# Optimization experiments

Hardware: AMD Instinct MI355X
Metric: run time of the kernel (lower is better)

## Reference

```python
import jax, jax.numpy as jnp
import numpy as np

D_MODEL = 128
D_INNER = 256   # expand=2
D_STATE = 16
DT_RANK = 8     # ceil(128/16)
D_CONV = 2
GROUPS = 4
EPS = 1e-5


def _mamba_dir(x, W_in, conv_w, conv_b, W_x, W_dt, b_dt, A_log, D, W_out):
    # x: [B, L, d_model]
    B, L, _ = x.shape
    xz = x @ W_in                               # [B, L, 2*d_inner]
    xp, z = xz[..., :D_INNER], xz[..., D_INNER:]
    # depthwise causal conv, kernel size 2 (pad-left 1)
    xprev = jnp.pad(xp, ((0, 0), (1, 0), (0, 0)))[:, :L]
    xc = jax.nn.silu(xprev * conv_w[:, 0] + xp * conv_w[:, 1] + conv_b)
    xdb = xc @ W_x                              # [B, L, dt_rank + 2*d_state]
    dt_r = xdb[..., :DT_RANK]
    Bc = xdb[..., DT_RANK:DT_RANK + D_STATE]    # [B, L, d_state]
    Cc = xdb[..., DT_RANK + D_STATE:]           # [B, L, d_state]
    dt = jax.nn.softplus(dt_r @ W_dt + b_dt)    # [B, L, d_inner]
    A = -jnp.exp(A_log)                         # [d_inner, d_state]

    def step(h, inp):
        dt_t, B_t, C_t, x_t = inp               # [B,di], [B,ds], [B,ds], [B,di]
        dA = jnp.exp(dt_t[:, :, None] * A)      # [B, di, ds]
        h = dA * h + (dt_t * x_t)[:, :, None] * B_t[:, None, :]
        y = jnp.einsum('bds,bs->bd', h, C_t)
        return h, y

    h0 = jnp.zeros((B, D_INNER, D_STATE), x.dtype)
    xs = (jnp.moveaxis(dt, 1, 0), jnp.moveaxis(Bc, 1, 0),
          jnp.moveaxis(Cc, 1, 0), jnp.moveaxis(xc, 1, 0))
    _, ys = jax.lax.scan(step, h0, xs)          # ys: [L, B, d_inner]
    y = jnp.moveaxis(ys, 0, 1) + D * xc
    y = y * jax.nn.silu(z)
    return y @ W_out                            # [B, L, d_model]


def _groupnorm_silu(x, gamma, beta):
    B, C, H, W = x.shape
    xg = x.reshape(B, GROUPS, C // GROUPS, H, W)
    mu = xg.mean(axis=(2, 3, 4), keepdims=True)
    var = xg.var(axis=(2, 3, 4), keepdims=True)
    xn = ((xg - mu) * jax.lax.rsqrt(var + EPS)).reshape(B, C, H, W)
    return jax.nn.silu(xn * gamma[None, :, None, None] + beta[None, :, None, None])


def setup_inputs() -> dict:
    key = jax.random.key(0)
    ks = jax.random.split(key, 24)
    s = 0.02
    A_log = jnp.log(jnp.tile(jnp.arange(1, D_STATE + 1, dtype=jnp.float32)[None, :], (D_INNER, 1)))
    inp = {"x": jax.random.normal(ks[0], (4, D_MODEL, 64, 64), jnp.float32)}
    for i, sfx in enumerate(("f", "b")):
        o = 1 + 9 * i
        inp[f"W_in_{sfx}"] = jax.random.normal(ks[o], (D_MODEL, 2 * D_INNER)) * s
        inp[f"conv_w_{sfx}"] = jax.random.normal(ks[o + 1], (D_INNER, D_CONV)) * 0.5
        inp[f"conv_b_{sfx}"] = jnp.zeros((D_INNER,))
        inp[f"W_x_{sfx}"] = jax.random.normal(ks[o + 2], (D_INNER, DT_RANK + 2 * D_STATE)) * s
        inp[f"W_dt_{sfx}"] = jax.random.normal(ks[o + 3], (DT_RANK, D_INNER)) * s
        inp[f"b_dt_{sfx}"] = jnp.full((D_INNER,), -3.0)
        inp[f"A_log_{sfx}"] = A_log
        inp[f"D_{sfx}"] = jnp.ones((D_INNER,))
        inp[f"W_out_{sfx}"] = jax.random.normal(ks[o + 4], (D_INNER, D_MODEL)) * s
    inp["gn_gamma"] = jnp.ones((D_MODEL,))
    inp["gn_beta"] = jnp.zeros((D_MODEL,))
    return inp


def reference(x, W_in_f, conv_w_f, conv_b_f, W_x_f, W_dt_f, b_dt_f, A_log_f, D_f, W_out_f,
              W_in_b, conv_w_b, conv_b_b, W_x_b, W_dt_b, b_dt_b, A_log_b, D_b, W_out_b,
              gn_gamma, gn_beta):
    B, C, H, W = x.shape
    xs = x.transpose(0, 2, 3, 1).reshape(B, H * W, C)
    y_f = _mamba_dir(xs, W_in_f, conv_w_f, conv_b_f, W_x_f, W_dt_f, b_dt_f, A_log_f, D_f, W_out_f)
    xr = xs[:, ::-1]
    y_b = _mamba_dir(xr, W_in_b, conv_w_b, conv_b_b, W_x_b, W_dt_b, b_dt_b, A_log_b, D_b, W_out_b)[:, ::-1]
    y = y_f + y_b                               # bidirectional combine
    y = y.reshape(B, H, W, C).transpose(0, 3, 1, 2)
    y = _groupnorm_silu(y, gn_gamma, gn_beta)
    return y + x
```

## Files before the change

### kernel.cpp

```cpp
#include <hip/hip_runtime.h>

#define Bn 4
#define Ln 4096
#define Cn 128
#define DIn 256
#define NCn 128
#define LCn 32
#define ROWS (Bn*Ln)

typedef short s8v __attribute__((ext_vector_type(8)));
typedef short s4v __attribute__((ext_vector_type(4)));
typedef unsigned short u8v __attribute__((ext_vector_type(8)));
typedef unsigned short u4v __attribute__((ext_vector_type(4)));
typedef float f4v __attribute__((ext_vector_type(4)));
typedef float f2v __attribute__((ext_vector_type(2)));

__device__ __forceinline__ float siluf(float x){ return x / (1.f + __expf(-x)); }
__device__ __forceinline__ unsigned short bfr(float f){
  uint u = __float_as_uint(f);
  return (unsigned short)((u + 0x7fffu + ((u>>16)&1u)) >> 16);
}
__device__ __forceinline__ float bf2f(unsigned short u){ return __uint_as_float(((uint)u)<<16); }

__device__ __forceinline__ void sp_w(float r, float& dtv, float& w){
  float e = __expf(-fabsf(r));
  float rc = 1.f / (1.f + e);
  dtv = fmaxf(r, 0.f) + __logf(1.f + e);
  w = (r > 0.f) ? e * rc : rc;
}

__device__ __forceinline__ int tile_off(int r, int gran, int ghalf){
  return ((r>>4)<<9) + ((r&15)<<5) + (((gran ^ ((r>>1)&3)))<<3) + ghalf;
}

#define SMEMB 18432

__global__ __launch_bounds__(256) void k_g1(const float* __restrict__ x,
    const float* __restrict__ Wf, const float* __restrict__ Wb,
    unsigned short* __restrict__ xpf, unsigned short* __restrict__ xpb,
    unsigned short* __restrict__ zbf, unsigned short* __restrict__ zbb)
{
  const int dir = blockIdx.z;
  const float* __restrict__ W = dir ? Wb : Wf;
  unsigned short* __restrict__ xp = dir ? xpb : xpf;
  unsigned short* __restrict__ zb = dir ? zbb : zbf;
  const int row0 = blockIdx.x * 128;
  const int n0 = blockIdx.y;
  const int b = row0 >> 12;
  const int t0 = row0 & (Ln-1);
  const float* __restrict__ xb = x + (size_t)b * Cn * Ln;

  __shared__ __align__(16) char smem[SMEMB];
  short* Ast = (short*)smem;
  short* Bst = (short*)smem + 8*512;
  float* Te  = (float*)smem;

  const int tid = threadIdx.x;
  const int lane = tid & 63;
  const int wid = tid >> 6;
  const int wr = wid >> 1, wc = wid & 1;
  const int r16 = lane & 15, kg = lane >> 4;

  const int q = tid & 31, kq = tid >> 5;
  const int kbase = 4*kq;
  const int g_true = kq >> 1;
  const int ghalf = (kq & 1) * 4;

  f4v acc[4][4];
  #pragma unroll
  for (int i=0;i<4;++i)
    #pragma unroll
    for (int j=0;j<4;++j) acc[i][j] = (f4v){0.f,0.f,0.f,0.f};

  float4 va[4], vb[4];
  {
    #pragma unroll
    for (int kk=0;kk<4;++kk) {
      va[kk] = (dir==0)
        ? *(const float4*)(xb + (size_t)(kbase+kk)*Ln + t0 + 4*q)
        : *(const float4*)(xb + (size_t)(kbase+kk)*Ln + (Ln-4 - t0 - 4*q));
      vb[kk] = *(const float4*)(W + (size_t)(kbase+kk)*512 + n0*128 + 4*q);
    }
  }
  for (int ks=0; ks<4; ++ks) {
    if (ks) __syncthreads();
    #pragma unroll
    for (int e=0;e<4;++e) {
      int r = 4*q + e;
      int off = tile_off(r, g_true, ghalf);
      int c = dir ? (3-e) : e;
      s4v hv;
      #pragma unroll
      for (int kk=0;kk<4;++kk) hv[kk] = (short)bfr(((const float*)&va[kk])[c]);
      *(s4v*)&Ast[off] = hv;
    }
    #pragma unroll
    for (int e=0;e<4;++e) {
      int r = 4*q + e;
      int off = tile_off(r, g_true, ghalf);
      s4v hv;
      #pragma unroll
      for (int kk=0;kk<4;++kk) hv[kk] = (short)bfr(((const float*)&vb[kk])[e]);
      *(s4v*)&Bst[off] = hv;
    }
    __syncthreads();
    if (ks < 3) {
      const int k0n = (ks+1)*32;
      #pragma unroll
      for (int kk=0;kk<4;++kk) {
        va[kk] = (dir==0)
          ? *(const float4*)(xb + (size_t)(k0n+kbase+kk)*Ln + t0 + 4*q)
          : *(const float4*)(xb + (size_t)(k0n+kbase+kk)*Ln + (Ln-4 - t0 - 4*q));
        vb[kk] = *(const float4*)(W + (size_t)(k0n+kbase+kk)*512 + n0*128 + 4*q);
      }
    }
    const int gsh = ((kg ^ ((r16>>1)&3)) << 3);
    s8v fa[4], fb[4];
    #pragma unroll
    for (int m=0;m<4;++m) fa[m] = *(const s8v*)&Ast[(wr*4+m)*512 + r16*32 + gsh];
    #pragma unroll
    for (int n=0;n<4;++n) fb[n] = *(const s8v*)&Bst[(wc*4+n)*512 + r16*32 + gsh];
    #pragma unroll
    for (int m=0;m<4;++m)
      #pragma unroll
      for (int n=0;n<4;++n)
        acc[m][n] = __builtin_amdgcn_mfma_f32_16x16x32_bf16(fa[m], fb[n], acc[m][n], 0,0,0);
  }
  __syncthreads();
  float* Tw = Te + wid*1088;
  #pragma unroll
  for (int m=0;m<4;++m) {
    #pragma unroll
    for (int n=0;n<4;++n)
      #pragma unroll
      for (int v=0;v<4;++v)
        Tw[(kg*4+v)*68 + n*16 + r16] = acc[m][n][v];
    #pragma unroll
    for (int rr=0;rr<4;++rr) {
      int r = rr*4 + (lane>>4);
      int c4 = lane & 15;
      float4 v4 = *(const float4*)&Tw[r*68 + c4*4];
      int row = row0 + wr*64 + m*16 + r;
      int colL = wc*64 + c4*4;
      u4v u; u[0]=bfr(v4.x); u[1]=bfr(v4.y); u[2]=bfr(v4.z); u[3]=bfr(v4.w);
      if (n0 < 2) {
        *(u4v*)(xp + (size_t)row*256 + n0*128 + colL) = u;
      } else {
        *(u4v*)(zb + (size_t)row*256 + (n0-2)*128 + colL) = u;
      }
    }
  }
}

__global__ __launch_bounds__(256) void k_conv(
    const unsigned short* __restrict__ xpf, const unsigned short* __restrict__ xpb,
    const float* __restrict__ cwf, const float* __restrict__ cwb,
    const float* __restrict__ cbf, const float* __restrict__ cbb,
    unsigned short* __restrict__ xcf, unsigned short* __restrict__ xcb)
{
  const int dir = blockIdx.y;
  const unsigned short* __restrict__ xpd = dir ? xpb : xpf;
  const float* __restrict__ cw = dir ? cwb : cwf;
  const float* __restrict__ cb = dir ? cbb : cbf;
  unsigned short* __restrict__ xc = dir ? xcb : xcf;
  const int n4 = ROWS * 64;
  for (int idx4 = blockIdx.x*256 + threadIdx.x; idx4 < n4; idx4 += gridDim.x*256) {
    int row = idx4 >> 6;
    int d0 = (idx4 & 63) * 4;
    u4v curu = *(const u4v*)(xpd + (size_t)row*256 + d0);
    u4v prevu = (u4v){0,0,0,0};
    if (row & (Ln-1)) prevu = *(const u4v*)(xpd + (size_t)(row-1)*256 + d0);
    float4 cwA = *(const float4*)(cw + d0*2);
    float4 cwB = *(const float4*)(cw + d0*2 + 4);
    float4 cb4 = *(const float4*)(cb + d0);
    u4v r;
    r[0] = bfr(siluf(fmaf(bf2f(prevu[0]),cwA.x, fmaf(bf2f(curu[0]),cwA.y, cb4.x))));
    r[1] = bfr(siluf(fmaf(bf2f(prevu[1]),cwA.z, fmaf(bf2f(curu[1]),cwA.w, cb4.y))));
    r[2] = bfr(siluf(fmaf(bf2f(prevu[2]),cwB.x, fmaf(bf2f(curu[2]),cwB.y, cb4.z))));
    r[3] = bfr(siluf(fmaf(bf2f(prevu[3]),cwB.z, fmaf(bf2f(curu[3]),cwB.w, cb4.w))));
    *(u4v*)(xc + (size_t)row*256 + d0) = r;
  }
}

__global__ __launch_bounds__(256) void k_g2(
    const unsigned short* __restrict__ xcf, const unsigned short* __restrict__ xcb,
    const float* __restrict__ Wxf, const float* __restrict__ Wxb,
    float* __restrict__ xdbf, float* __restrict__ xdbb)
{
  const int dir = blockIdx.z;
  const unsigned short* __restrict__ xc = dir ? xcb : xcf;
  const float* __restrict__ Wx = dir ? Wxb : Wxf;
  float* __restrict__ xdb = dir ? xdbb : xdbf;
  const int row0 = blockIdx.x * 64;

  __shared__ __align__(16) short Ast[4*512];
  __shared__ __align__(16) short Bst[4*512];

  const int tid = threadIdx.x;
  const int lane = tid & 63;
  const int wid = tid >> 6;
  const int wr = wid >> 1, wc = wid & 1;
  const int r16 = lane & 15, kg = lane >> 4;
  const int ar = tid >> 2, ag = tid & 3;
  const int bn = tid & 63, bg = tid >> 6;

  f4v acc[2][2];
  #pragma unroll
  for (int i=0;i<2;++i)
    #pragma unroll
    for (int j=0;j<2;++j) acc[i][j] = (f4v){0.f,0.f,0.f,0.f};

  for (int ks=0; ks<8; ++ks) {
    const int k0 = ks*32;
    if (ks) __syncthreads();
    {
      u8v u = *(const u8v*)(xc + (size_t)(row0+ar)*256 + k0 + ag*8);
      *(u8v*)&Ast[tile_off(ar, ag, 0)] = u;
    }
    {
      s8v hv;
      #pragma unroll
      for (int i=0;i<8;++i) {
        int k = k0 + bg*8 + i;
        float f = (bn < 40) ? Wx[(size_t)k*40 + bn] : 0.f;
        hv[i] = (short)bfr(f);
      }
      *(s8v*)&Bst[tile_off(bn, bg, 0)] = hv;
    }
    __syncthreads();
    const int gsh = ((kg ^ ((r16>>1)&3)) << 3);
    s8v fa[2], fb[2];
    #pragma unroll
    for (int m=0;m<2;++m) fa[m] = *(const s8v*)&Ast[(wr*2+m)*512 + r16*32 + gsh];
    #pragma unroll
    for (int n=0;n<2;++n) fb[n] = *(const s8v*)&Bst[(wc*2+n)*512 + r16*32 + gsh];
    #pragma unroll
    for (int m=0;m<2;++m)
      #pragma unroll
      for (int n=0;n<2;++n)
        acc[m][n] = __builtin_amdgcn_mfma_f32_16x16x32_bf16(fa[m], fb[n], acc[m][n], 0,0,0);
  }
  #pragma unroll
  for (int m=0;m<2;++m)
    #pragma unroll
    for (int n=0;n<2;++n) {
      int col = wc*32 + n*16 + r16;
      if (col < 40) {
        #pragma unroll
        for (int v=0;v<4;++v) {
          int row = row0 + wr*32 + m*16 + kg*4 + v;
          xdb[(size_t)row*40 + col] = acc[m][n][v];
        }
      }
    }
}

__global__ __launch_bounds__(128,4) void k_pass1(
    const float* __restrict__ xdbf, const float* __restrict__ xdbb,
    const unsigned short* __restrict__ xcf, const unsigned short* __restrict__ xcb,
    const float* __restrict__ Wdtf, const float* __restrict__ Wdtb,
    const float* __restrict__ bdtf, const float* __restrict__ bdtb,
    const float* __restrict__ Alf, const float* __restrict__ Alb,
    float* __restrict__ sdtf, float* __restrict__ sdtb,
    float* __restrict__ hkf, float* __restrict__ hkb)
{
  const int dir = blockIdx.y;
  const float* __restrict__ xdb = dir ? xdbb : xdbf;
  const unsigned short* __restrict__ xc = dir ? xcb : xcf;
  const float* __restrict__ Wdt = dir ? Wdtb : Wdtf;
  const float* __restrict__ bdt = dir ? bdtb : bdtf;
  const float* __restrict__ Al  = dir ? Alb  : Alf;
  float* __restrict__ sdt = dir ? sdtb : sdtf;
  float* __restrict__ hk  = dir ? hkb  : hkf;
  const int dh = blockIdx.x & 1;
  const int cc = blockIdx.x >> 1;
  const int b = cc >> 7, c = cc & 127;
  const int t0 = c * LCn;
  __shared__ float S[LCn*32];
  const int tid = threadIdx.x;
  #pragma unroll
  for (int j=0;j<6;++j) {
    int idx = tid + j*128;
    int t = idx/24, jj = idx - t*24;
    S[t*32 + jj] = xdb[(size_t)(b*Ln + t0 + t)*40 + jj];
  }
  const int d = dh*128 + tid;
  float Areg[16];
  bool st = true;
  #pragma unroll
  for (int s=0;s<16;++s) {
    Areg[s] = -__expf(Al[d*16+s]);
    st = st && (fabsf(Areg[s] + (float)(s+1)) <= 3e-5f*(float)(s+1));
  }
  f2v wdt2[4];
  #pragma unroll
  for (int j=0;j<4;++j) wdt2[j] = (f2v){Wdt[(2*j)*256+d], Wdt[(2*j+1)*256+d]};
  const float bd = bdt[d];
  f2v h2[8];
  #pragma unroll
  for (int i=0;i<8;++i) h2[i] = (f2v){0.f,0.f};
  float sacc = 0.f;
  const unsigned short* xcp = xc + (size_t)(b*Ln + t0)*256 + d;
  __syncthreads();
  if (st) {
    for (int t=0;t<LCn;++t) {
      float4 sA = *(const float4*)&S[t*32];
      float4 sB = *(const float4*)&S[t*32+4];
      f2v r2 = (f2v){sA.x,sA.y}*wdt2[0] + (f2v){sA.z,sA.w}*wdt2[1];
      r2 = (f2v){sB.x,sB.y}*wdt2[2] + r2;
      r2 = (f2v){sB.z,sB.w}*wdt2[3] + r2;
      float rr = bd + r2.x + r2.y;
      float dtv, wv;
      sp_w(rr, dtv, wv);
      float4 b0 = *(const float4*)&S[t*32+8];
      float4 b1 = *(const float4*)&S[t*32+12];
      float4 b2 = *(const float4*)&S[t*32+16];
      float4 b3 = *(const float4*)&S[t*32+20];
      float xv = bf2f(xcp[(size_t)t*256]);
      float u = dtv * xv;
      sacc += dtv;
      float w2s = wv*wv;
      float w4 = w2s*w2s, w8 = w4*w4;
      f2v wstep = (f2v){w2s, w2s};
      f2v wpa = (f2v){wv, w2s};
      f2v wpb = wpa * (f2v){w8, w8};
      f2v u2 = (f2v){u, u};
      h2[0] = h2[0]*wpa + u2*(f2v){b0.x,b0.y}; wpa *= wstep;
      h2[4] = h2[4]*wpb + u2*(f2v){b2.x,b2.y}; wpb *= wstep;
      h2[1] = h2[1]*wpa + u2*(f2v){b0.z,b0.w}; wpa *= wstep;
      h2[5] = h2[5]*wpb + u2*(f2v){b2.z,b2.w}; wpb *= wstep;
      h2[2] = h2[2]*wpa + u2*(f2v){b1.x,b1.y}; wpa *= wstep;
      h2[6] = h2[6]*wpb + u2*(f2v){b3.x,b3.y}; wpb *= wstep;
      h2[3] = h2[3]*wpa + u2*(f2v){b1.z,b1.w};
      h2[7] = h2[7]*wpb + u2*(f2v){b3.z,b3.w};
    }
  } else {
    for (int t=0;t<LCn;++t) {
      float4 sA = *(const float4*)&S[t*32];
      float4 sB = *(const float4*)&S[t*32+4];
      float rr = bd;
      rr = fmaf(sA.x,wdt2[0].x, fmaf(sA.y,wdt2[0].y, fmaf(sA.z,wdt2[1].x, fmaf(sA.w,wdt2[1].y, rr))));
      rr = fmaf(sB.x,wdt2[2].x, fmaf(sB.y,wdt2[2].y, fmaf(sB.z,wdt2[3].x, fmaf(sB.w,wdt2[3].y, rr))));
      float dtv, wv;
      sp_w(rr, dtv, wv);
      float bq[16];
      #pragma unroll
      for (int i=0;i<4;++i) *(float4*)&bq[4*i] = *(const float4*)&S[t*32 + 8 + 4*i];
      float xv = bf2f(xcp[(size_t)t*256]);
      float u = dtv * xv;
      sacc += dtv;
      #pragma unroll
      for (int s=0;s<16;++s) {
        float hv = (s&1) ? h2[s>>1].y : h2[s>>1].x;
        hv = fmaf(hv, __expf(dtv*Areg[s]), u*bq[s]);
        if (s&1) h2[s>>1].y = hv; else h2[s>>1].x = hv;
      }
    }
  }
  sdt[(size_t)(b*NCn + c)*256 + d] = sacc;
  #pragma unroll
  for (int i=0;i<8;++i) {
    hk[(size_t)((b*NCn + c)*16 + 2*i)*256 + d]   = h2[i].x;
    hk[(size_t)((b*NCn + c)*16 + 2*i+1)*256 + d] = h2[i].y;
  }
}

__global__ __launch_bounds__(256) void k_pass2(
    const float* __restrict__ Alf, const float* __restrict__ Alb,
    const float* __restrict__ sdtf, const float* __restrict__ sdtb,
    float* __restrict__ hkf, float* __restrict__ hkb)
{
  const int dir = blockIdx.y;
  const float* __restrict__ Al  = dir ? Alb : Alf;
  const float* __restrict__ sdt = dir ? sdtb : sdtf;
  float* __restrict__ hk = dir ? hkb : hkf;
  int g = blockIdx.x*256 + threadIdx.x;
  int d = g & 255, s = (g >> 8) & 15, b = g >> 12;
  float Ad = -__expf(Al[d*16+s]);
  float h = 0.f;
  float sd_n = sdt[(size_t)(b*NCn)*256 + d];
  size_t hi_n = (size_t)((b*NCn)*16 + s)*256 + d;
  float he_n = hk[hi_n];
  for (int c=0;c<NCn;++c) {
    float sd = sd_n, he = he_n;
    size_t hi = hi_n;
    if (c+1 < NCn) {
      int bc = b*NCn + c + 1;
      sd_n = sdt[(size_t)bc*256 + d];
      hi_n = (size_t)(bc*16 + s)*256 + d;
      he_n = hk[hi_n];
    }
    hk[hi] = h;
    h = fmaf(__expf(Ad*sd), h, he);
  }
}

__global__ __launch_bounds__(128,4) void k_pass3(
    const float* __restrict__ xdbf, const float* __restrict__ xdbb,
    const unsigned short* __restrict__ xcf, const unsigned short* __restrict__ xcb,
    const float* __restrict__ Wdtf, const float* __restrict__ Wdtb,
    const float* __restrict__ bdtf, const float* __restrict__ bdtb,
    const float* __restrict__ Alf, const float* __restrict__ Alb,
    const float* __restrict__ Dvf, const float* __restrict__ Dvb,
    const float* __restrict__ hkf, const float* __restrict__ hkb,
    const unsigned short* __restrict__ zbf, const unsigned short* __restrict__ zbb,
    unsigned short* __restrict__ ygf, unsigned short* __restrict__ ygb)
{
  const int dir = blockIdx.y;
  const float* __restrict__ xdb = dir ? xdbb : xdbf;
  const unsigned short* __restrict__ xc = dir ? xcb : xcf;
  const float* __restrict__ Wdt = dir ? Wdtb : Wdtf;
  const float* __restrict__ bdt = dir ? bdtb : bdtf;
  const float* __restrict__ Al  = dir ? Alb  : Alf;
  const float* __restrict__ Dv  = dir ? Dvb  : Dvf;
  const float* __restrict__ hk  = dir ? hkb  : hkf;
  const unsigned short* __restrict__ zbd = dir ? zbb : zbf;
  unsigned short* __restrict__ yg = dir ? ygb : ygf;
  const int dh = blockIdx.x & 1;
  const int cc = blockIdx.x >> 1;
  const int b = cc >> 7, c = cc & 127;
  const int t0 = c * LCn;
  __shared__ float S[LCn*48];
  const int tid = threadIdx.x;
  #pragma unroll
  for (int j=0;j<10;++j) {
    int idx = tid + j*128;
    int t = idx/40, jj = idx - t*40;
    S[t*48 + jj] = xdb[(size_t)(b*Ln + t0 + t)*40 + jj];
  }
  const int d = dh*128 + tid;
  float Areg[16];
  bool st = true;
  #pragma unroll
  for (int s=0;s<16;++s) {
    Areg[s] = -__expf(Al[d*16+s]);
    st = st && (fabsf(Areg[s] + (float)(s+1)) <= 3e-5f*(float)(s+1));
  }
  f2v wdt2[4];
  #pragma unroll
  for (int j=0;j<4;++j) wdt2[j] = (f2v){Wdt[(2*j)*256+d], Wdt[(2*j+1)*256+d]};
  const float bd = bdt[d];
  const float Dd = Dv[d];
  f2v h2[8];
  #pragma unroll
  for (int i=0;i<8;++i)
    h2[i] = (f2v){hk[(size_t)((b*NCn + c)*16 + 2*i)*256 + d],
                  hk[(size_t)((b*NCn + c)*16 + 2*i+1)*256 + d]};
  const unsigned short* xcp = xc + (size_t)(b*Ln + t0)*256 + d;
  const unsigned short* zbp = zbd + (size_t)(b*Ln + t0)*256 + d;
  unsigned short* ygp = yg + (size_t)(b*Ln + t0)*256 + d;
  __syncthreads();
  if (st) {
    for (int t=0;t<LCn;++t) {
      float4 sA = *(const float4*)&S[t*48];
      float4 sB = *(const float4*)&S[t*48+4];
      f2v r2 = (f2v){sA.x,sA.y}*wdt2[0] + (f2v){sA.z,sA.w}*wdt2[1];
      r2 = (f2v){sB.x,sB.y}*wdt2[2] + r2;
      r2 = (f2v){sB.z,sB.w}*wdt2[3] + r2;
      float rr = bd + r2.x + r2.y;
      float dtv, wv;
      sp_w(rr, dtv, wv);
      float4 b0 = *(const float4*)&S[t*48+8];
      float4 b1 = *(const float4*)&S[t*48+12];
      float4 b2 = *(const float4*)&S[t*48+16];
      float4 b3 = *(const float4*)&S[t*48+20];
      float4 c0 = *(const float4*)&S[t*48+24];
      float4 c1 = *(const float4*)&S[t*48+28];
      float4 c2 = *(const float4*)&S[t*48+32];
      float4 c3 = *(const float4*)&S[t*48+36];
      float xv = bf2f(xcp[(size_t)t*256]);
      float u = dtv * xv;
      float w2s = wv*wv;
      float w4 = w2s*w2s, w8 = w4*w4;
      f2v wstep = (f2v){w2s, w2s};
      f2v wpa = (f2v){wv, w2s};
      f2v wpb = wpa * (f2v){w8, w8};
      f2v u2 = (f2v){u, u};
      f2v yA = (f2v){0.f,0.f}, yB = (f2v){0.f,0.f};
      h2[0] = h2[0]*wpa + u2*(f2v){b0.x,b0.y}; yA = h2[0]*(f2v){c0.x,c0.y} + yA; wpa *= wstep;
      h2[4] = h2[4]*wpb + u2*(f2v){b2.x,b2.y}; yB = h2[4]*(f2v){c2.x,c2.y} + yB; wpb *= wstep;
      h2[1] = h2[1]*wpa + u2*(f2v){b0.z,b0.w}; yA = h2[1]*(f2v){c0.z,c0.w} + yA; wpa *= wstep;
      h2[5] = h2[5]*wpb + u2*(f2v){b2.z,b2.w}; yB = h2[5]*(f2v){c2.z,c2.w} + yB; wpb *= wstep;
      h2[2] = h2[2]*wpa + u2*(f2v){b1.x,b1.y}; yA = h2[2]*(f2v){c1.x,c1.y} + yA; wpa *= wstep;
      h2[6] = h2[6]*wpb + u2*(f2v){b3.x,b3.y}; yB = h2[6]*(f2v){c3.x,c3.y} + yB; wpb *= wstep;
      h2[3] = h2[3]*wpa + u2*(f2v){b1.z,b1.w}; yA = h2[3]*(f2v){c1.z,c1.w} + yA;
      h2[7] = h2[7]*wpb + u2*(f2v){b3.z,b3.w}; yB = h2[7]*(f2v){c3.z,c3.w} + yB;
      float y = yA.x + yA.y + yB.x + yB.y;
      y = fmaf(Dd, xv, y);
      float zv = bf2f(zbp[(size_t)t*256]);
      ygp[(size_t)t*256] = bfr(y * siluf(zv));
    }
  } else {
    for (int t=0;t<LCn;++t) {
      float4 sA = *(const float4*)&S[t*48];
      float4 sB = *(const float4*)&S[t*48+4];
      float rr = bd;
      rr = fmaf(sA.x,wdt2[0].x, fmaf(sA.y,wdt2[0].y, fmaf(sA.z,wdt2[1].x, fmaf(sA.w,wdt2[1].y, rr))));
      rr = fmaf(sB.x,wdt2[2].x, fmaf(sB.y,wdt2[2].y, fmaf(sB.z,wdt2[3].x, fmaf(sB.w,wdt2[3].y, rr))));
      float dtv, wv;
      sp_w(rr, dtv, wv);
      float bq[16], cq[16];
      #pragma unroll
      for (int i=0;i<4;++i) {
        *(float4*)&bq[4*i] = *(const float4*)&S[t*48 + 8 + 4*i];
        *(float4*)&cq[4*i] = *(const float4*)&S[t*48 + 24 + 4*i];
      }
      float xv = bf2f(xcp[(size_t)t*256]);
      float u = dtv * xv;
      float y = 0.f;
      #pragma unroll
      for (int s=0;s<16;++s) {
        float hv = (s&1) ? h2[s>>1].y : h2[s>>1].x;
        hv = fmaf(hv, __expf(dtv*Areg[s]), u*bq[s]);
        if (s&1) h2[s>>1].y = hv; else h2[s>>1].x = hv;
        y = fmaf(hv, cq[s], y);
      }
      y = fmaf(Dd, xv, y);
      float zv = bf2f(zbp[(size_t)t*256]);
      ygp[(size_t)t*256] = bfr(y * siluf(zv));
    }
  }
}

__global__ __launch_bounds__(256) void k_gout(
    const unsigned short* __restrict__ ygf, const unsigned short* __restrict__ ygb,
    const float* __restrict__ Wof, const float* __restrict__ Wob,
    float* __restrict__ yp)
{
  const int row0 = blockIdx.x * 128;
  const int khalf = blockIdx.y;
  const int dir = blockIdx.z;
  const unsigned short* __restrict__ ygd = dir ? ygb : ygf;
  const float* __restrict__ Wod = dir ? Wob : Wof;
  float* __restrict__ ypart = yp + (size_t)(dir*2 + khalf) * ROWS * 128;
  const int b = row0 >> 12;
  const int l0 = row0 & (Ln-1);

  __shared__ __align__(16) char smem[SMEMB];
  short* Ast = (short*)smem;
  short* Bst = (short*)smem + 8*512;
  float* Te  = (float*)smem;

  const int tid = threadIdx.x;
  const int lane = tid & 63;
  const int wid = tid >> 6;
  const int wr = wid >> 1, wc = wid & 1;
  const int r16 = lane & 15, kg = lane >> 4;

  const int ar = tid >> 1, kh = tid & 1;
  const int q = tid & 31, kq = tid >> 5;
  const int kbase = 4*kq;
  const int g_true = kq >> 1;
  const int ghalf = (kq & 1) * 4;

  f4v acc[4][4];
  #pragma unroll
  for (int i=0;i<4;++i)
    #pragma unroll
    for (int j=0;j<4;++j) acc[i][j] = (f4v){0.f,0.f,0.f,0.f};

  for (int ks=0; ks<4; ++ks) {
    const int kk0 = khalf*128 + ks*32;
    if (ks) __syncthreads();
    {
      int rl = l0 + ar;
      size_t srow = (size_t)b*Ln + (dir ? (Ln-1-rl) : rl);
      const unsigned short* s = ygd + srow*256 + kk0 + kh*16;
      u8v u0 = *(const u8v*)(s);
      u8v u1 = *(const u8v*)(s + 8);
      int o0 = tile_off(ar, 2*kh,   0);
      int o1 = tile_off(ar, 2*kh+1, 0);
      *(u8v*)&Ast[o0] = u0;
      *(u8v*)&Ast[o1] = u1;
    }
    {
      float4 vb[4];
      #pragma unroll
      for (int kk=0;kk<4;++kk)
        vb[kk] = *(const float4*)(Wod + (size_t)(kk0+kbase+kk)*128 + 4*q);
      #pragma unroll
      for (int e=0;e<4;++e) {
        int r = 4*q + e;
        int off = tile_off(r, g_true, ghalf);
        s4v hv;
        #pragma unroll
        for (int kk=0;kk<4;++kk) hv[kk] = (short)bfr(((const float*)&vb[kk])[e]);
        *(s4v*)&Bst[off] = hv;
      }
    }
    __syncthreads();
    const int gsh = ((kg ^ ((r16>>1)&3)) << 3);
    s8v fa[4], fb[4];
    #pragma unroll
    for (int m=0;m<4;++m) fa[m] = *(const s8v*)&Ast[(wr*4+m)*512 + r16*32 + gsh];
    #pragma unroll
    for (int n=0;n<4;++n) fb[n] = *(const s8v*)&Bst[(wc*4+n)*512 + r16*32 + gsh];
    #pragma unroll
    for (int m=0;m<4;++m)
      #pragma unroll
      for (int n=0;n<4;++n)
        acc[m][n] = __builtin_amdgcn_mfma_f32_16x16x32_bf16(fa[m], fb[n], acc[m][n], 0,0,0);
  }
  __syncthreads();
  float* Tw = Te + wid*1088;
  #pragma unroll
  for (int m=0;m<4;++m) {
    #pragma unroll
    for (int n=0;n<4;++n)
      #pragma unroll
      for (int v=0;v<4;++v)
        Tw[(kg*4+v)*68 + n*16 + r16] = acc[m][n][v];
    #pragma unroll
    for (int rr=0;rr<4;++rr) {
      int r = rr*4 + (lane>>4);
      int c4 = lane & 15;
      float4 v4 = *(const float4*)&Tw[r*68 + c4*4];
      int row = row0 + wr*64 + m*16 + r;
      *(float4*)(ypart + (size_t)row*128 + wc*64 + c4*4) = v4;
    }
  }
}

__global__ __launch_bounds__(256) void k_gnstat(const float* __restrict__ yp,
    float* __restrict__ ysum, float* __restrict__ part)
{
  const int bg = blockIdx.x >> 4;
  const int blk = blockIdx.x & 15;
  const int b = bg >> 2, g = bg & 3;
  const size_t P = (size_t)ROWS*128;
  float s=0.f, q=0.f;
  #pragma unroll
  for (int i=0;i<8;++i) {
    int e4 = blk*2048 + threadIdx.x + i*256;
    int l = e4 >> 3, c4 = e4 & 7;
    size_t base = (size_t)(b*Ln + l)*128 + g*32 + c4*4;
    float4 v0 = *(const float4*)(yp + base);
    float4 v1 = *(const float4*)(yp + P + base);
    float4 v2 = *(const float4*)(yp + 2*P + base);
    float4 v3 = *(const float4*)(yp + 3*P + base);
    float4 v;
    v.x = v0.x+v1.x+v2.x+v3.x;
    v.y = v0.y+v1.y+v2.y+v3.y;
    v.z = v0.z+v1.z+v2.z+v3.z;
    v.w = v0.w+v1.w+v2.w+v3.w;
    *(float4*)(ysum + base) = v;
    s += v.x+v.y+v.z+v.w;
    q = fmaf(v.x,v.x, fmaf(v.y,v.y, fmaf(v.z,v.z, fmaf(v.w,v.w, q))));
  }
  __shared__ float rs[256], rq[256];
  rs[threadIdx.x]=s; rq[threadIdx.x]=q;
  __syncthreads();
  for (int off=128; off>0; off>>=1) {
    if (threadIdx.x < off) { rs[threadIdx.x]+=rs[threadIdx.x+off]; rq[threadIdx.x]+=rq[threadIdx.x+off]; }
    __syncthreads();
  }
  if (threadIdx.x==0) { part[blockIdx.x*2]=rs[0]; part[blockIdx.x*2+1]=rq[0]; }
}

__global__ void k_gnred(const float* __restrict__ part, float* __restrict__ mr)
{
  int t = threadIdx.x;
  if (t < 16) {
    float s=0.f,q=0.f;
    for (int k=0;k<16;++k){ s+=part[(t*16+k)*2]; q+=part[(t*16+k)*2+1]; }
    const float inv = 1.f/131072.f;
    float mean = s*inv;
    float var = fmaf(-mean, mean, q*inv);
    mr[t*2] = mean;
    mr[t*2+1] = rsqrtf(var + 1e-5f);
  }
}

__global__ __launch_bounds__(256) void k_gnapply(const float* __restrict__ ysum,
    const float* __restrict__ mr, const float* __restrict__ gamma, const float* __restrict__ beta,
    const float* __restrict__ x, float* __restrict__ out)
{
  const int b = blockIdx.x >> 6;
  const int l0 = (blockIdx.x & 63) * 64;
  __shared__ float T[64][132];
  const int tid = threadIdx.x;
  #pragma unroll
  for (int j=0;j<8;++j) {
    int f = tid + j*256;
    int l = f >> 5, c4 = f & 31;
    *(float4*)&T[l][c4*4] = *(const float4*)(ysum + (size_t)(b*Ln + l0 + l)*128 + c4*4);
  }
  __syncthreads();
  #pragma unroll
  for (int j=0;j<8;++j) {
    int f = tid + j*256;
    int c = f >> 4, lv = f & 15;
    int bg = b*4 + (c>>5);
    float mean = mr[bg*2];
    float rstd = mr[bg*2+1];
    float gam = gamma[c], bet = beta[c];
    size_t base = (size_t)(b*Cn + c)*Ln + l0 + lv*4;
    float4 xv = *(const float4*)(x + base);
    float4 r;
    r.x = siluf(fmaf((T[lv*4+0][c]-mean)*rstd, gam, bet)) + xv.x;
    r.y = siluf(fmaf((T[lv*4+1][c]-mean)*rstd, gam, bet)) + xv.y;
    r.z = siluf(fmaf((T[lv*4+2][c]-mean)*rstd, gam, bet)) + xv.z;
    r.w = siluf(fmaf((T[lv*4+3][c]-mean)*rstd, gam, bet)) + xv.w;
    *(float4*)(out + base) = r;
  }
}

extern "C" void kernel_launch(void* const* d_in, const int* in_sizes, int n_in,
                              void* d_out, int out_size, void* d_ws, size_t ws_size,
                              hipStream_t stream) {
  const float* x      = (const float*)d_in[0];
  const float* W_in_f = (const float*)d_in[1];
  const float* cw_f   = (const float*)d_in[2];
  const float* cb_f   = (const float*)d_in[3];
  const float* Wx_f   = (const float*)d_in[4];
  const float* Wdt_f  = (const float*)d_in[5];
  const float* bdt_f  = (const float*)d_in[6];
  const float* Al_f   = (const float*)d_in[7];
  const float* D_f    = (const float*)d_in[8];
  const float* Wo_f   = (const float*)d_in[9];
  const float* W_in_b = (const float*)d_in[10];
  const float* cw_b   = (const float*)d_in[11];
  const float* cb_b   = (const float*)d_in[12];
  const float* Wx_b   = (const float*)d_in[13];
  const float* Wdt_b  = (const float*)d_in[14];
  const float* bdt_b  = (const float*)d_in[15];
  const float* Al_b   = (const float*)d_in[16];
  const float* D_b    = (const float*)d_in[17];
  const float* Wo_b   = (const float*)d_in[18];
  const float* gamma  = (const float*)d_in[19];
  const float* beta   = (const float*)d_in[20];
  float* out = (float*)d_out;

  float* w = (float*)d_ws;
  size_t o = 0;
  float* xpr0 = w + o; o += (size_t)ROWS*256;
  float* xpr1 = w + o; o += (size_t)ROWS*256;
  unsigned short* xc0 = (unsigned short*)(w + o); o += (size_t)ROWS*128;
  unsigned short* xc1 = (unsigned short*)(w + o); o += (size_t)ROWS*128;
  unsigned short* zb0 = (unsigned short*)(w + o); o += (size_t)ROWS*128;
  unsigned short* zb1 = (unsigned short*)(w + o); o += (size_t)ROWS*128;
  unsigned short* yg0 = (unsigned short*)(w + o); o += (size_t)ROWS*128;
  unsigned short* yg1 = (unsigned short*)(w + o); o += (size_t)ROWS*128;
  float* xdb0 = w + o; o += (size_t)ROWS*40;
  float* xdb1 = w + o; o += (size_t)ROWS*40;
  float* sdt0 = w + o; o += (size_t)Bn*NCn*256;
  float* sdt1 = w + o; o += (size_t)Bn*NCn*256;
  float* hk0  = w + o; o += (size_t)Bn*NCn*16*256;
  float* hk1  = w + o; o += (size_t)Bn*NCn*16*256;
  float* part = w + o; o += 512;
  float* mr   = w + o; o += 32;
  unsigned short* xp0 = (unsigned short*)xpr0;
  unsigned short* xp1 = (unsigned short*)xpr1;
  float* yp   = xpr0;
  float* ysum = xdb0;
  if (ws_size < o*sizeof(float)) return;

  k_g1<<<dim3(ROWS/128, 4, 2), 256, 0, stream>>>(x, W_in_f, W_in_b, xp0, xp1, zb0, zb1);
  k_conv<<<dim3(1024, 2), 256, 0, stream>>>(xp0, xp1, cw_f, cw_b, cb_f, cb_b, xc0, xc1);
  k_g2<<<dim3(ROWS/64, 1, 2), 256, 0, stream>>>(xc0, xc1, Wx_f, Wx_b, xdb0, xdb1);
  k_pass1<<<dim3(Bn*NCn*2, 2), 128, 0, stream>>>(xdb0, xdb1, xc0, xc1, Wdt_f, Wdt_b,
                                                 bdt_f, bdt_b, Al_f, Al_b, sdt0, sdt1, hk0, hk1);
  k_pass2<<<dim3(64, 2), 256, 0, stream>>>(Al_f, Al_b, sdt0, sdt1, hk0, hk1);
  k_pass3<<<dim3(Bn*NCn*2, 2), 128, 0, stream>>>(xdb0, xdb1, xc0, xc1, Wdt_f, Wdt_b,
                                                 bdt_f, bdt_b, Al_f, Al_b, D_f, D_b,
                                                 hk0, hk1, zb0, zb1, yg0, yg1);
  k_gout<<<dim3(ROWS/128, 2, 2), 256, 0, stream>>>(yg0, yg1, Wo_f, Wo_b, yp);
  k_gnstat<<<dim3(256), 256, 0, stream>>>(yp, ysum, part);
  k_gnred<<<dim3(1), 64, 0, stream>>>(part, mr);
  k_gnapply<<<dim3(256), 256, 0, stream>>>(ysum, mr, gamma, beta, x, out);
}
```

Before: 146.7 us.

## Fuse both scan directions into one output GEMM accumulation and halve partial buffers

The output projection kernel now accumulates the forward and backward directions in the same accumulator by looping over eight K-steps, so it writes two partial-sum planes instead of four. Row tiles shrink from 128 to 64, which keeps the grid size the same while lowering per-thread accumulator registers. The group-norm stats kernel now reads two partial planes instead of four, cutting global memory traffic for the fp32 intermediates. An extra barrier is added inside the epilogue loop, and each block now does twice as many K iterations with more B-tile conversion work per output row.

New measurement: 144.9 us. No clear change (-1.2%).

```diff
diff --git a/kernel.cpp b/kernel.cpp
--- a/kernel.cpp
+++ b/kernel.cpp
@@ -527,18 +527,15 @@
     const float* __restrict__ Wof, const float* __restrict__ Wob,
     float* __restrict__ yp)
 {
-  const int row0 = blockIdx.x * 128;
+  const int row0 = blockIdx.x * 64;
   const int khalf = blockIdx.y;
-  const int dir = blockIdx.z;
-  const unsigned short* __restrict__ ygd = dir ? ygb : ygf;
-  const float* __restrict__ Wod = dir ? Wob : Wof;
-  float* __restrict__ ypart = yp + (size_t)(dir*2 + khalf) * ROWS * 128;
+  float* __restrict__ ypart = yp + (size_t)khalf * ROWS * 128;
   const int b = row0 >> 12;
   const int l0 = row0 & (Ln-1);
 
   __shared__ __align__(16) char smem[SMEMB];
   short* Ast = (short*)smem;
-  short* Bst = (short*)smem + 8*512;
+  short* Bst = (short*)smem + 4*512;
   float* Te  = (float*)smem;
 
   const int tid = threadIdx.x;
@@ -547,31 +544,29 @@
   const int wr = wid >> 1, wc = wid & 1;
   const int r16 = lane & 15, kg = lane >> 4;
 
-  const int ar = tid >> 1, kh = tid & 1;
+  const int ar = tid >> 2, ag = tid & 3;
   const int q = tid & 31, kq = tid >> 5;
   const int kbase = 4*kq;
   const int g_true = kq >> 1;
   const int ghalf = (kq & 1) * 4;
 
-  f4v acc[4][4];
-  #pragma unroll
-  for (int i=0;i<4;++i)
+  f4v acc[2][4];
+  #pragma unroll
+  for (int i=0;i<2;++i)
     #pragma unroll
     for (int j=0;j<4;++j) acc[i][j] = (f4v){0.f,0.f,0.f,0.f};
 
-  for (int ks=0; ks<4; ++ks) {
-    const int kk0 = khalf*128 + ks*32;
+  for (int ks=0; ks<8; ++ks) {
+    const int dir = ks >> 2;
+    const int kk0 = khalf*128 + (ks & 3)*32;
+    const unsigned short* __restrict__ ygd = dir ? ygb : ygf;
+    const float* __restrict__ Wod = dir ? Wob : Wof;
     if (ks) __syncthreads();
     {
       int rl = l0 + ar;
       size_t srow = (size_t)b*Ln + (dir ? (Ln-1-rl) : rl);
-      const unsigned short* s = ygd + srow*256 + kk0 + kh*16;
-      u8v u0 = *(const u8v*)(s);
-      u8v u1 = *(const u8v*)(s + 8);
-      int o0 = tile_off(ar, 2*kh,   0);
-      int o1 = tile_off(ar, 2*kh+1, 0);
-      *(u8v*)&Ast[o0] = u0;
-      *(u8v*)&Ast[o1] = u1;
+      u8v u = *(const u8v*)(ygd + srow*256 + kk0 + ag*8);
+      *(u8v*)&Ast[tile_off(ar, ag, 0)] = u;
     }
     {
       float4 vb[4];
@@ -590,13 +585,13 @@
     }
     __syncthreads();
     const int gsh = ((kg ^ ((r16>>1)&3)) << 3);
-    s8v fa[4], fb[4];
-    #pragma unroll
-    for (int m=0;m<4;++m) fa[m] = *(const s8v*)&Ast[(wr*4+m)*512 + r16*32 + gsh];
+    s8v fa[2], fb[4];
+    #pragma unroll
+    for (int m=0;m<2;++m) fa[m] = *(const s8v*)&Ast[(wr*2+m)*512 + r16*32 + gsh];
     #pragma unroll
     for (int n=0;n<4;++n) fb[n] = *(const s8v*)&Bst[(wc*4+n)*512 + r16*32 + gsh];
     #pragma unroll
-    for (int m=0;m<4;++m)
+    for (int m=0;m<2;++m)
       #pragma unroll
       for (int n=0;n<4;++n)
         acc[m][n] = __builtin_amdgcn_mfma_f32_16x16x32_bf16(fa[m], fb[n], acc[m][n], 0,0,0);
@@ -604,7 +599,7 @@
   __syncthreads();
   float* Tw = Te + wid*1088;
   #pragma unroll
-  for (int m=0;m<4;++m) {
+  for (int m=0;m<2;++m) {
     #pragma unroll
     for (int n=0;n<4;++n)
       #pragma unroll
@@ -615,9 +610,10 @@
       int r = rr*4 + (lane>>4);
       int c4 = lane & 15;
       float4 v4 = *(const float4*)&Tw[r*68 + c4*4];
-      int row = row0 + wr*64 + m*16 + r;
+      int row = row0 + wr*32 + m*16 + r;
       *(float4*)(ypart + (size_t)row*128 + wc*64 + c4*4) = v4;
     }
+    __syncthreads();
   }
 }
 
@@ -636,13 +632,11 @@
     size_t base = (size_t)(b*Ln + l)*128 + g*32 + c4*4;
     float4 v0 = *(const float4*)(yp + base);
     float4 v1 = *(const float4*)(yp + P + base);
-    float4 v2 = *(const float4*)(yp + 2*P + base);
-    float4 v3 = *(const float4*)(yp + 3*P + base);
     float4 v;
-    v.x = v0.x+v1.x+v2.x+v3.x;
-    v.y = v0.y+v1.y+v2.y+v3.y;
-    v.z = v0.z+v1.z+v2.z+v3.z;
-    v.w = v0.w+v1.w+v2.w+v3.w;
+    v.x = v0.x+v1.x;
+    v.y = v0.y+v1.y;
+    v.z = v0.z+v1.z;
+    v.w = v0.w+v1.w;
     *(float4*)(ysum + base) = v;
     s += v.x+v.y+v.z+v.w;
     q = fmaf(v.x,v.x, fmaf(v.y,v.y, fmaf(v.z,v.z, fmaf(v.w,v.w, q))));
@@ -764,7 +758,7 @@
   k_pass3<<<dim3(Bn*NCn*2, 2), 128, 0, stream>>>(xdb0, xdb1, xc0, xc1, Wdt_f, Wdt_b,
                                                  bdt_f, bdt_b, Al_f, Al_b, D_f, D_b,
                                                  hk0, hk1, zb0, zb1, yg0, yg1);
-  k_gout<<<dim3(ROWS/128, 2, 2), 256, 0, stream>>>(yg0, yg1, Wo_f, Wo_b, yp);
+  k_gout<<<dim3(ROWS/64, 2), 256, 0, stream>>>(yg0, yg1, Wo_f, Wo_b, yp);
   k_gnstat<<<dim3(256), 256, 0, stream>>>(yp, ysum, part);
   k_gnred<<<dim3(1), 64, 0, stream>>>(part, mr);
   k_gnapply<<<dim3(256), 256, 0, stream>>>(ysum, mr, gamma, beta, x, out);
```
